# Kernel tuning notes

Hardware: AMD Instinct MI355X
Metric: run time of the kernel (lower is better)

The kernel has to match this reference:

```python
import jax, jax.numpy as jnp
import numpy as np

STATE_LEN = 128

def _layernorm(x, eps=1e-5):
    m = jnp.mean(x, axis=-1, keepdims=True)
    v = jnp.mean(jnp.square(x - m), axis=-1, keepdims=True)
    return (x - m) * jax.lax.rsqrt(v + eps)

def setup_inputs() -> dict:
    key = jax.random.key(0)
    ks = jax.random.split(key, 20)
    B, S, L = 2, 2048, STATE_LEN
    Din, Dk, Dv, H = 1024, 64, 64, 8
    T = S + 2 * L  # 2304
    x = jax.random.normal(ks[0], (B, T, Din), jnp.float32)
    def w(k, dout):
        return jax.random.normal(k, (H, Din, dout), jnp.float32) / np.sqrt(Din).astype(np.float32)
    inp = {
        'x': x,
        'ln_g':  1.0 + 0.02 * jax.random.normal(ks[1], (H, Din), jnp.float32),
        'ln_b':  0.02 * jax.random.normal(ks[2], (H, Din), jnp.float32),
        'ln_gs': 1.0 + 0.02 * jax.random.normal(ks[3], (H, Din), jnp.float32),
        'ln_bs': 0.02 * jax.random.normal(ks[4], (H, Din), jnp.float32),
        'ln_ge': 1.0 + 0.02 * jax.random.normal(ks[5], (H, Din), jnp.float32),
        'ln_be': 0.02 * jax.random.normal(ks[6], (H, Din), jnp.float32),
        'Wq':   w(ks[7], Dk),  'Wk':   w(ks[8], Dk),  'Wv':   w(ks[9], Dv),
        'Wq_s': w(ks[10], Dk), 'Wk_s': w(ks[11], Dk), 'Wv_s': w(ks[12], Dv),
        'Wq_e': w(ks[13], Dk), 'Wk_e': w(ks[14], Dk), 'Wv_e': w(ks[15], Dv),
        'offset': 0,
    }
    return inp

def _forward(x, ln_g, ln_b, ln_gs, ln_bs, ln_ge, ln_be,
             Wq, Wk, Wv, Wq_s, Wk_s, Wv_s, Wq_e, Wk_e, Wv_e):
    L = STATE_LEN
    B, T, Din = x.shape
    # extract_state: start state, middle sequence, end state
    xs, xm, xe = x[:, :L], x[:, L:T - L], x[:, T - L:]
    # LayerNorm stats are parameter-free; per-head affine applied after
    ns, nm, ne = _layernorm(xs), _layernorm(xm), _layernorm(xe)
    def aff(n, g, b):  # [B,seg,Din] -> [B,H,seg,Din]
        return n[:, None, :, :] * g[None, :, None, :] + b[None, :, None, :]
    hs, hm, he = aff(ns, ln_gs, ln_bs), aff(nm, ln_g, ln_b), aff(ne, ln_ge, ln_be)
    proj = lambda h, W: jnp.einsum('bhsd,hde->bhse', h, W)
    q = jnp.concatenate([proj(hs, Wq_s), proj(hm, Wq), proj(he, Wq_e)], axis=2)
    k = jnp.concatenate([proj(hs, Wk_s), proj(hm, Wk), proj(he, Wk_e)], axis=2)
    v = jnp.concatenate([proj(hs, Wv_s), proj(hm, Wv), proj(he, Wv_e)], axis=2)
    Dk = q.shape[-1]
    scores = jnp.einsum('bhsd,bhtd->bhst', q, k) / jnp.asarray(np.sqrt(Dk), q.dtype)
    # Faithful to the torch code: a FLOAT tril-of-ones mask is passed to SDPA,
    # which ADDS it to the scores (it does not set -inf anywhere).
    mask = jnp.tril(jnp.ones((T, T), scores.dtype))
    att = jax.nn.softmax(scores + mask, axis=-1)
    out = jnp.einsum('bhst,bhtd->bhsd', att, v)  # [B,H,T,Dv]
    H, Dv = out.shape[1], out.shape[3]
    # torch.concat over heads on last dim
    return out.transpose(0, 2, 1, 3).reshape(B, T, H * Dv)

def reference(x, ln_g, ln_b, ln_gs, ln_bs, ln_ge, ln_be,
              Wq, Wk, Wv, Wq_s, Wk_s, Wv_s, Wq_e, Wk_e, Wv_e, offset):
    # offset unused: position_embedders are None in this configuration
    return _forward(x, ln_g, ln_b, ln_gs, ln_bs, ln_ge, ln_be,
                    Wq, Wk, Wv, Wq_s, Wk_s, Wv_s, Wq_e, Wk_e, Wv_e)
```

## Files before the change

### kernel.cpp

```cpp
#include <hip/hip_runtime.h>

#define TSEQ 2304
#define DIN  1024
#define NH   8
#define DD   64
#define NC   1536
#define MROWS 4608
#define L2E  1.44269504f
#define EF   2.71828183f

typedef __attribute__((ext_vector_type(8))) short bf16x8;
typedef __attribute__((ext_vector_type(4))) float f32x4;
typedef __attribute__((ext_vector_type(4))) unsigned short u16x4;

__device__ __forceinline__ unsigned short f2bf(float f){
    union { float f; unsigned int u; } x; x.f = f;
    unsigned int r = x.u + 0x7FFFu + ((x.u >> 16) & 1u);
    return (unsigned short)(r >> 16);
}

__device__ __forceinline__ unsigned int pack_bf2(float a, float b){
    union { float f; unsigned int u; } xa, xb;
    xa.f = a; xb.f = b;
    return __builtin_amdgcn_perm(xb.u + 0x8000u, xa.u + 0x8000u, 0x07060302u);
}

__device__ __forceinline__ void gload_lds16(const void* g, void* l){
    __builtin_amdgcn_global_load_lds(
        (const __attribute__((address_space(1))) void*)g,
        (__attribute__((address_space(3))) void*)l, 16, 0, 0);
}

struct WArgs {
    const float* W[9];
    const float* g[3];
    const float* bv[3];
};

__global__ __launch_bounds__(256) void k_pre(WArgs a, const float* __restrict__ x,
                                             unsigned short* __restrict__ wb,
                                             float* __restrict__ bias,
                                             unsigned short* __restrict__ nrm)
{
    __shared__ float lds[64][65];
    __shared__ float red[4][64];
    __shared__ float r1[4], r2[4];
    const int bid = blockIdx.x;
    const int tid = threadIdx.x;
    if (bid < 1152){
        const int dt = bid & 15, h = (bid >> 4) & 7, sp = bid >> 7;
        const int seg = sp / 3, proj = sp % 3;
        const float* W = a.W[seg*3 + proj];
        const float* g = a.g[seg];
        const int d0 = dt * 64;
        {
            const int e = tid & 63, rq = tid >> 6;
#pragma unroll
            for (int rr = 0; rr < 16; ++rr){
                const int dl = rr*4 + rq;
                lds[dl][e] = W[((size_t)h*DIN + d0 + dl)*DD + e];
            }
        }
        __syncthreads();
        {
            const int dl = tid & 63, eq = tid >> 6;
            const int n0 = proj*512 + h*64;
            const float gv = g[h*DIN + d0 + dl];
#pragma unroll
            for (int rr = 0; rr < 16; ++rr){
                const int el = eq*16 + rr;
                wb[((size_t)seg*NC + n0 + el)*DIN + d0 + dl] = f2bf(lds[dl][el] * gv);
            }
        }
    } else if (bid < 1224){
        const int u = bid - 1152;
        const int h = u & 7, sp = u >> 3;
        const int seg = sp / 3, proj = sp % 3;
        const float* W  = a.W[seg*3 + proj];
        const float* bv = a.bv[seg];
        const int e = tid & 63, dc = tid >> 6;
        float sum = 0.f;
        for (int i = 0; i < 256; ++i){
            const int d = dc*256 + i;
            sum += bv[h*DIN + d] * W[((size_t)h*DIN + d)*DD + e];
        }
        red[dc][e] = sum;
        __syncthreads();
        if (dc == 0)
            bias[seg*NC + proj*512 + h*64 + e] = red[0][e] + red[1][e] + red[2][e] + red[3][e];
    } else {
        const int row = bid - 1224;
        const float* xr = x + (size_t)row * DIN;
        f32x4 v = *(const f32x4*)&xr[tid*4];
        float s1 = v[0]+v[1]+v[2]+v[3];
        float s2 = v[0]*v[0]+v[1]*v[1]+v[2]*v[2]+v[3]*v[3];
#pragma unroll
        for (int m = 1; m < 64; m <<= 1){ s1 += __shfl_xor(s1, m); s2 += __shfl_xor(s2, m); }
        const int wid = tid >> 6;
        if ((tid & 63) == 0){ r1[wid] = s1; r2[wid] = s2; }
        __syncthreads();
        s1 = r1[0]+r1[1]+r1[2]+r1[3];
        s2 = r2[0]+r2[1]+r2[2]+r2[3];
        const float mean = s1 * (1.f/1024.f);
        const float var  = s2 * (1.f/1024.f) - mean*mean;
        const float rstd = rsqrtf(var + 1e-5f);
        u16x4 ov;
#pragma unroll
        for (int j = 0; j < 4; ++j) ov[j] = f2bf((v[j]-mean)*rstd);
        *(u16x4*)&nrm[(size_t)row*DIN + tid*4] = ov;
    }
}

__global__ __launch_bounds__(256) void k_gemm(
    const unsigned short* __restrict__ A,
    const unsigned short* __restrict__ Wb,
    const float* __restrict__ bias,
    unsigned short* __restrict__ qo,
    unsigned short* __restrict__ ko,
    unsigned short* __restrict__ vt)
{
    __shared__ unsigned short As[128*32];
    __shared__ unsigned short Bs[128*32];
    const int mt = blockIdx.x, nt = blockIdx.y;
    const int row0 = mt*128, n0 = nt*128;
    const int rloc = row0 % TSEQ;
    const int seg = (rloc < 128) ? 0 : (rloc < 2176 ? 1 : 2);
    const unsigned short* Bp = Wb + (size_t)seg * NC * DIN;
    const int tid = threadIdx.x;
    const int wid = tid >> 6, lane = tid & 63;
    const int wr = wid >> 1, wc = wid & 1;
    const int lr = lane & 15, lg = lane >> 4;
    const int srow = lane >> 2;
    const int selem = (lane & 3) * 8;
    f32x4 acc[4][4];
#pragma unroll
    for (int m = 0; m < 4; ++m)
#pragma unroll
        for (int n = 0; n < 4; ++n) acc[m][n] = (f32x4){0.f,0.f,0.f,0.f};

    for (int kt = 0; kt < DIN/32; ++kt){
        const int k0 = kt*32;
        __syncthreads();
#pragma unroll
        for (int i = 0; i < 2; ++i){
            const int c = wid*2 + i;
            const int r = c*16 + srow;
            gload_lds16(&A [(size_t)(row0 + r)*DIN + k0 + selem], &As[c*512]);
            gload_lds16(&Bp[(size_t)(n0  + r)*DIN + k0 + selem], &Bs[c*512]);
        }
        __syncthreads();
        bf16x8 af[4], bfr[4];
#pragma unroll
        for (int m = 0; m < 4; ++m) af[m]  = *(const bf16x8*)&As[(wr*64 + m*16 + lr)*32 + lg*8];
#pragma unroll
        for (int n = 0; n < 4; ++n) bfr[n] = *(const bf16x8*)&Bs[(wc*64 + n*16 + lr)*32 + lg*8];
#pragma unroll
        for (int m = 0; m < 4; ++m)
#pragma unroll
            for (int n = 0; n < 4; ++n)
                acc[m][n] = __builtin_amdgcn_mfma_f32_16x16x32_bf16(af[m], bfr[n], acc[m][n], 0, 0, 0);
    }
    const int b_ = row0 / TSEQ;
    const int t0 = row0 - b_ * TSEQ;
#pragma unroll
    for (int m = 0; m < 4; ++m){
#pragma unroll
        for (int n = 0; n < 4; ++n){
            const int nglob = n0 + wc*64 + n*16 + lr;
            const float bs = bias[seg*NC + nglob];
            const int proj = nglob >> 9, hh = (nglob >> 6) & 7, e = nglob & 63;
            if (proj < 2){
                unsigned short* op = (proj == 0) ? qo : ko;
                const float scale = (proj == 0) ? 0.125f * L2E : 1.0f;
                const size_t ob = ((size_t)(b_*NH + hh) * TSEQ) * DD + e;
#pragma unroll
                for (int j = 0; j < 4; ++j){
                    const int t = t0 + wr*64 + m*16 + 4*lg + j;
                    op[ob + (size_t)t * DD] = f2bf((acc[m][n][j] + bs) * scale);
                }
            } else {
                unsigned short* vp = vt + ((size_t)(b_*NH + hh)*DD + e)*TSEQ;
                const int t = t0 + wr*64 + m*16 + 4*lg;
                u16x4 pk;
#pragma unroll
                for (int j = 0; j < 4; ++j) pk[j] = f2bf(acc[m][n][j] + bs);
                *(u16x4*)&vp[t] = pk;
            }
        }
    }
}

__global__ __launch_bounds__(256) void k_attn(
    const unsigned short* __restrict__ Q,
    const unsigned short* __restrict__ K,
    const unsigned short* __restrict__ Vt,
    float* __restrict__ po0,
    float* __restrict__ po1,
    float* __restrict__ out2,
    float* __restrict__ pl)
{
    __shared__ unsigned short Ks[2][64*64];
    __shared__ unsigned short Vs[2][64*64];
    __shared__ unsigned short Plds[4][16][72];
    const int qt = blockIdx.x;
    const int bh = blockIdx.y;
    const int z  = blockIdx.z;
    const int kt0 = z*12, kt1 = kt0 + 12;
    const int tid  = threadIdx.x;
    const int w    = tid >> 6;
    const int lane = tid & 63;
    const int lr = lane & 15, lg = lane >> 4;
    const size_t qkb = (size_t)bh * TSEQ * DD;
    const size_t vtb = (size_t)bh * DD * TSEQ;
    const int q0 = qt*64 + w*16;
    const int qr = q0 + lr;

    const int rsub = lane >> 3;
    const int cgx  = (lane & 7) ^ rsub;
    const char* Kbase  = (const char*)(K  + qkb);
    const char* Vtbase = (const char*)(Vt + vtb);

    bf16x8 aq[2];
#pragma unroll
    for (int ks = 0; ks < 2; ++ks)
        aq[ks] = *(const bf16x8*)&Q[qkb + (size_t)(q0 + lr)*DD + ks*32 + lg*8];

    float lsum = 0.f;
    f32x4 o[4];
#pragma unroll
    for (int nd = 0; nd < 4; ++nd) o[nd] = (f32x4){0.f,0.f,0.f,0.f};

    auto stage = [&](int kt, int b){
        const int kn = kt*64;
#pragma unroll
        for (int i = 0; i < 2; ++i){
            const int c = w*2 + i;
            const int r = c*8 + rsub;
            gload_lds16(Kbase  + (size_t)(kn + r)*128 + cgx*16,              &Ks[b][c*512]);
            gload_lds16(Vtbase + (size_t)r*(TSEQ*2) + (size_t)kn*2 + cgx*16, &Vs[b][c*512]);
        }
    };

    stage(kt0, 0);
    __syncthreads();

    unsigned int* PldsW = (unsigned int*)&Plds[w][0][0];

    int buf = 0;
    for (int kt = kt0; kt < kt1; ++kt){
        const int kc0 = kt*64;
        if (kt + 1 < kt1) stage(kt + 1, buf ^ 1);
        f32x4 s[4];
#pragma unroll
        for (int ns = 0; ns < 4; ++ns) s[ns] = (f32x4){0.f,0.f,0.f,0.f};
#pragma unroll
        for (int ks = 0; ks < 2; ++ks){
#pragma unroll
            for (int ns = 0; ns < 4; ++ns){
                bf16x8 bk = *(const bf16x8*)&Ks[buf][(ns*16 + lr)*64 + (((4*ks + lg) ^ (lr & 7))*8)];
                s[ns] = __builtin_amdgcn_mfma_f32_16x16x32_bf16(bk, aq[ks], s[ns], 0, 0, 0);
            }
        }
        if (kt == qt){
            lsum *= EF;
#pragma unroll
            for (int nd = 0; nd < 4; ++nd)
#pragma unroll
                for (int j = 0; j < 4; ++j) o[nd][j] *= EF;
#pragma unroll
            for (int ns = 0; ns < 4; ++ns){
                const int kb = kc0 + ns*16 + 4*lg;
                float p0 = exp2f(s[ns][0] + ((kb + 0 <= qr) ? L2E : 0.f));
                float p1 = exp2f(s[ns][1] + ((kb + 1 <= qr) ? L2E : 0.f));
                float p2 = exp2f(s[ns][2] + ((kb + 2 <= qr) ? L2E : 0.f));
                float p3 = exp2f(s[ns][3] + ((kb + 3 <= qr) ? L2E : 0.f));
                lsum += (p0 + p1) + (p2 + p3);
                PldsW[lr*36 + ns*8 + 2*lg + 0] = pack_bf2(p0, p1);
                PldsW[lr*36 + ns*8 + 2*lg + 1] = pack_bf2(p2, p3);
            }
        } else {
#pragma unroll
            for (int ns = 0; ns < 4; ++ns){
                float p0 = exp2f(s[ns][0]);
                float p1 = exp2f(s[ns][1]);
                float p2 = exp2f(s[ns][2]);
                float p3 = exp2f(s[ns][3]);
                lsum += (p0 + p1) + (p2 + p3);
                PldsW[lr*36 + ns*8 + 2*lg + 0] = pack_bf2(p0, p1);
                PldsW[lr*36 + ns*8 + 2*lg + 1] = pack_bf2(p2, p3);
            }
        }
#pragma unroll
        for (int ks = 0; ks < 2; ++ks){
            bf16x8 pa = *(const bf16x8*)&Plds[w][lr][ks*32 + lg*8];
#pragma unroll
            for (int nd = 0; nd < 4; ++nd){
                bf16x8 bv = *(const bf16x8*)&Vs[buf][(nd*16 + lr)*64 + (((4*ks + lg) ^ (lr & 7))*8)];
                o[nd] = __builtin_amdgcn_mfma_f32_16x16x32_bf16(pa, bv, o[nd], 0, 0, 0);
            }
        }
        __syncthreads();
        buf ^= 1;
    }
    if (qt >= kt1){
        lsum *= EF;
#pragma unroll
        for (int nd = 0; nd < 4; ++nd)
#pragma unroll
            for (int j = 0; j < 4; ++j) o[nd][j] *= EF;
    }
    lsum += __shfl_xor(lsum, 16);
    lsum += __shfl_xor(lsum, 32);
    const int tix = (z*16 + bh)*36 + qt;
    if (lg == 0) pl[tix*64 + w*16 + lr] = lsum;
    const int rowb = w*16 + 4*lg;
    if (z < 2){
        float* po = (z == 0) ? po0 : po1;
        const size_t tb = (size_t)(bh*36 + qt) * 4096;
#pragma unroll
        for (int j = 0; j < 4; ++j)
#pragma unroll
            for (int nd = 0; nd < 4; ++nd)
                po[tb + (size_t)(rowb + j)*64 + nd*16 + lr] = o[nd][j];
    } else {
        const int b_ = bh >> 3, hh = bh & 7;
#pragma unroll
        for (int j = 0; j < 4; ++j){
            const int t = qt*64 + rowb + j;
            const size_t ob = ((size_t)(b_*TSEQ + t))*512 + hh*64;
#pragma unroll
            for (int nd = 0; nd < 4; ++nd)
                out2[ob + nd*16 + lr] = o[nd][j];
        }
    }
}

__global__ __launch_bounds__(256) void k_comb(
    const float* __restrict__ po0, const float* __restrict__ po1,
    const float* __restrict__ pl, float* __restrict__ out)
{
    const int qt = blockIdx.x, bh = blockIdx.y;
    const int b_ = bh >> 3, hh = bh & 7;
    const int tid = threadIdx.x;
    const int row = tid >> 2;
    const int c0  = (tid & 3) * 16;
    const int t0ix = bh*36 + qt;
    const float inv = 1.0f / (pl[t0ix*64 + row] + pl[(576 + t0ix)*64 + row] + pl[(1152 + t0ix)*64 + row]);
    const size_t tb = (size_t)t0ix * 4096 + row*64 + c0;
    const size_t ob = ((size_t)b_*TSEQ + qt*64 + row)*512 + hh*64 + c0;
#pragma unroll
    for (int i = 0; i < 4; ++i){
        f32x4 a = *(const f32x4*)&po0[tb + i*4];
        f32x4 b = *(const f32x4*)&po1[tb + i*4];
        f32x4 c = *(const f32x4*)&out[ob + i*4];
        f32x4 r;
#pragma unroll
        for (int j = 0; j < 4; ++j) r[j] = (a[j] + b[j] + c[j]) * inv;
        *(f32x4*)&out[ob + i*4] = r;
    }
}

extern "C" void kernel_launch(void* const* d_in, const int* in_sizes, int n_in,
                              void* d_out, int out_size, void* d_ws, size_t ws_size,
                              hipStream_t stream)
{
    const float* x     = (const float*)d_in[0];
    const float* ln_g  = (const float*)d_in[1];
    const float* ln_b  = (const float*)d_in[2];
    const float* ln_gs = (const float*)d_in[3];
    const float* ln_bs = (const float*)d_in[4];
    const float* ln_ge = (const float*)d_in[5];
    const float* ln_be = (const float*)d_in[6];
    const float* Wq    = (const float*)d_in[7];
    const float* Wk    = (const float*)d_in[8];
    const float* Wv    = (const float*)d_in[9];
    const float* Wq_s  = (const float*)d_in[10];
    const float* Wk_s  = (const float*)d_in[11];
    const float* Wv_s  = (const float*)d_in[12];
    const float* Wq_e  = (const float*)d_in[13];
    const float* Wk_e  = (const float*)d_in[14];
    const float* Wv_e  = (const float*)d_in[15];

    uint8_t* w = (uint8_t*)d_ws;
    unsigned short* nrm = (unsigned short*)(w);
    unsigned short* wb  = (unsigned short*)(w + 9437184);
    float*          bia = (float*)        (w + 18874368);
    unsigned short* q_  = (unsigned short*)(w + 18892800);
    unsigned short* k_  = (unsigned short*)(w + 23611392);
    unsigned short* vt_ = (unsigned short*)(w + 28329984);
    float*          pl  = (float*)        (w + 33048576);
    float*          po0 = (float*)        (w);
    float*          po1 = (float*)        (w + 9437184);

    WArgs wa;
    wa.W[0] = Wq_s; wa.W[1] = Wk_s; wa.W[2] = Wv_s;
    wa.W[3] = Wq;   wa.W[4] = Wk;   wa.W[5] = Wv;
    wa.W[6] = Wq_e; wa.W[7] = Wk_e; wa.W[8] = Wv_e;
    wa.g[0] = ln_gs; wa.g[1] = ln_g; wa.g[2] = ln_ge;
    wa.bv[0] = ln_bs; wa.bv[1] = ln_b; wa.bv[2] = ln_be;

    float* out = (float*)d_out;
    k_pre <<<dim3(5832),      dim3(256), 0, stream>>>(wa, x, wb, bia, nrm);
    k_gemm<<<dim3(36, 12),    dim3(256), 0, stream>>>(nrm, wb, bia, q_, k_, vt_);
    k_attn<<<dim3(36, 16, 3), dim3(256), 0, stream>>>(q_, k_, vt_, po0, po1, out, pl);
    k_comb<<<dim3(36, 16),    dim3(256), 0, stream>>>(po0, po1, pl, out);
}
```

Measured before the change: 109.9 us.

## Double query rows per wave, split keys four ways, combine partials via atomics

Each wave now handles 32 query rows instead of 16, so every K/V tile loaded into LDS is reused across twice as many queries. The key range is split into four chunks of 9 tiles instead of three of 12. Partial outputs are accumulated straight into the zeroed output with float atomicAdd rather than through separate partial buffers, leaving only a per-row normalisation pass. The P packing uses the hardware v_cvt_pk_bf16_f32 instruction. In exchange the change adds a memset, atomic traffic, extra register pressure and a non-deterministic summation order.

```diff
diff --git a/kernel.cpp b/kernel.cpp
--- a/kernel.cpp
+++ b/kernel.cpp
@@ -19,10 +19,10 @@
     return (unsigned short)(r >> 16);
 }
 
-__device__ __forceinline__ unsigned int pack_bf2(float a, float b){
-    union { float f; unsigned int u; } xa, xb;
-    xa.f = a; xb.f = b;
-    return __builtin_amdgcn_perm(xb.u + 0x8000u, xa.u + 0x8000u, 0x07060302u);
+__device__ __forceinline__ unsigned int cvtpk(float a, float b){
+    unsigned int r;
+    asm("v_cvt_pk_bf16_f32 %0, %1, %2" : "=v"(r) : "v"(a), "v"(b));
+    return r;
 }
 
 __device__ __forceinline__ void gload_lds16(const void* g, void* l){
@@ -194,41 +194,43 @@
     const unsigned short* __restrict__ Q,
     const unsigned short* __restrict__ K,
     const unsigned short* __restrict__ Vt,
-    float* __restrict__ po0,
-    float* __restrict__ po1,
-    float* __restrict__ out2,
+    float* __restrict__ out,
     float* __restrict__ pl)
 {
     __shared__ unsigned short Ks[2][64*64];
     __shared__ unsigned short Vs[2][64*64];
-    __shared__ unsigned short Plds[4][16][72];
-    const int qt = blockIdx.x;
-    const int bh = blockIdx.y;
-    const int z  = blockIdx.z;
-    const int kt0 = z*12, kt1 = kt0 + 12;
+    __shared__ unsigned short Plds[4][32][72];
+    const int qtb = blockIdx.x;
+    const int bh  = blockIdx.y;
+    const int z   = blockIdx.z;
+    const int kt0 = z*9, kt1 = kt0 + 9;
     const int tid  = threadIdx.x;
     const int w    = tid >> 6;
     const int lane = tid & 63;
     const int lr = lane & 15, lg = lane >> 4;
     const size_t qkb = (size_t)bh * TSEQ * DD;
     const size_t vtb = (size_t)bh * DD * TSEQ;
-    const int q0 = qt*64 + w*16;
-    const int qr = q0 + lr;
+    const int q0w = qtb*128 + w*32;
+    const int kd  = qtb*2 + (w >> 1);
 
     const int rsub = lane >> 3;
     const int cgx  = (lane & 7) ^ rsub;
     const char* Kbase  = (const char*)(K  + qkb);
     const char* Vtbase = (const char*)(Vt + vtb);
 
-    bf16x8 aq[2];
-#pragma unroll
-    for (int ks = 0; ks < 2; ++ks)
-        aq[ks] = *(const bf16x8*)&Q[qkb + (size_t)(q0 + lr)*DD + ks*32 + lg*8];
-
-    float lsum = 0.f;
-    f32x4 o[4];
-#pragma unroll
-    for (int nd = 0; nd < 4; ++nd) o[nd] = (f32x4){0.f,0.f,0.f,0.f};
+    bf16x8 aq[2][2];
+#pragma unroll
+    for (int qg = 0; qg < 2; ++qg)
+#pragma unroll
+        for (int ks = 0; ks < 2; ++ks)
+            aq[qg][ks] = *(const bf16x8*)&Q[qkb + (size_t)(q0w + qg*16 + lr)*DD + ks*32 + lg*8];
+
+    float lsum[2] = {0.f, 0.f};
+    f32x4 o[2][4];
+#pragma unroll
+    for (int qg = 0; qg < 2; ++qg)
+#pragma unroll
+        for (int nd = 0; nd < 4; ++nd) o[qg][nd] = (f32x4){0.f,0.f,0.f,0.f};
 
     auto stage = [&](int kt, int b){
         const int kn = kt*64;
@@ -250,113 +252,134 @@
     for (int kt = kt0; kt < kt1; ++kt){
         const int kc0 = kt*64;
         if (kt + 1 < kt1) stage(kt + 1, buf ^ 1);
-        f32x4 s[4];
-#pragma unroll
-        for (int ns = 0; ns < 4; ++ns) s[ns] = (f32x4){0.f,0.f,0.f,0.f};
-#pragma unroll
-        for (int ks = 0; ks < 2; ++ks){
-#pragma unroll
-            for (int ns = 0; ns < 4; ++ns){
-                bf16x8 bk = *(const bf16x8*)&Ks[buf][(ns*16 + lr)*64 + (((4*ks + lg) ^ (lr & 7))*8)];
-                s[ns] = __builtin_amdgcn_mfma_f32_16x16x32_bf16(bk, aq[ks], s[ns], 0, 0, 0);
-            }
-        }
-        if (kt == qt){
-            lsum *= EF;
+        bf16x8 bk[2][4];
+#pragma unroll
+        for (int ks = 0; ks < 2; ++ks)
+#pragma unroll
+            for (int ns = 0; ns < 4; ++ns)
+                bk[ks][ns] = *(const bf16x8*)&Ks[buf][(ns*16 + lr)*64 + (((4*ks + lg) ^ (lr & 7))*8)];
+        f32x4 s[2][4];
+#pragma unroll
+        for (int qg = 0; qg < 2; ++qg)
+#pragma unroll
+            for (int ns = 0; ns < 4; ++ns) s[qg][ns] = (f32x4){0.f,0.f,0.f,0.f};
+#pragma unroll
+        for (int qg = 0; qg < 2; ++qg)
+#pragma unroll
+            for (int ks = 0; ks < 2; ++ks)
+#pragma unroll
+                for (int ns = 0; ns < 4; ++ns)
+                    s[qg][ns] = __builtin_amdgcn_mfma_f32_16x16x32_bf16(bk[ks][ns], aq[qg][ks], s[qg][ns], 0, 0, 0);
+        if (kt == kd){
+#pragma unroll
+            for (int qg = 0; qg < 2; ++qg){
+                lsum[qg] *= EF;
+#pragma unroll
+                for (int nd = 0; nd < 4; ++nd)
+#pragma unroll
+                    for (int j = 0; j < 4; ++j) o[qg][nd][j] *= EF;
+                const int qr = q0w + qg*16 + lr;
+#pragma unroll
+                for (int ns = 0; ns < 4; ++ns){
+                    const int kb = kc0 + ns*16 + 4*lg;
+                    float p0 = exp2f(s[qg][ns][0] + ((kb + 0 <= qr) ? L2E : 0.f));
+                    float p1 = exp2f(s[qg][ns][1] + ((kb + 1 <= qr) ? L2E : 0.f));
+                    float p2 = exp2f(s[qg][ns][2] + ((kb + 2 <= qr) ? L2E : 0.f));
+                    float p3 = exp2f(s[qg][ns][3] + ((kb + 3 <= qr) ? L2E : 0.f));
+                    lsum[qg] += (p0 + p1) + (p2 + p3);
+                    PldsW[(qg*16 + lr)*36 + ns*8 + 2*lg + 0] = cvtpk(p0, p1);
+                    PldsW[(qg*16 + lr)*36 + ns*8 + 2*lg + 1] = cvtpk(p2, p3);
+                }
+            }
+        } else {
+#pragma unroll
+            for (int qg = 0; qg < 2; ++qg){
+#pragma unroll
+                for (int ns = 0; ns < 4; ++ns){
+                    float p0 = exp2f(s[qg][ns][0]);
+                    float p1 = exp2f(s[qg][ns][1]);
+                    float p2 = exp2f(s[qg][ns][2]);
+                    float p3 = exp2f(s[qg][ns][3]);
+                    lsum[qg] += (p0 + p1) + (p2 + p3);
+                    PldsW[(qg*16 + lr)*36 + ns*8 + 2*lg + 0] = cvtpk(p0, p1);
+                    PldsW[(qg*16 + lr)*36 + ns*8 + 2*lg + 1] = cvtpk(p2, p3);
+                }
+            }
+        }
+        bf16x8 bv[2][4];
+#pragma unroll
+        for (int ks = 0; ks < 2; ++ks)
 #pragma unroll
             for (int nd = 0; nd < 4; ++nd)
-#pragma unroll
-                for (int j = 0; j < 4; ++j) o[nd][j] *= EF;
-#pragma unroll
-            for (int ns = 0; ns < 4; ++ns){
-                const int kb = kc0 + ns*16 + 4*lg;
-                float p0 = exp2f(s[ns][0] + ((kb + 0 <= qr) ? L2E : 0.f));
-                float p1 = exp2f(s[ns][1] + ((kb + 1 <= qr) ? L2E : 0.f));
-                float p2 = exp2f(s[ns][2] + ((kb + 2 <= qr) ? L2E : 0.f));
-                float p3 = exp2f(s[ns][3] + ((kb + 3 <= qr) ? L2E : 0.f));
-                lsum += (p0 + p1) + (p2 + p3);
-                PldsW[lr*36 + ns*8 + 2*lg + 0] = pack_bf2(p0, p1);
-                PldsW[lr*36 + ns*8 + 2*lg + 1] = pack_bf2(p2, p3);
-            }
-        } else {
-#pragma unroll
-            for (int ns = 0; ns < 4; ++ns){
-                float p0 = exp2f(s[ns][0]);
-                float p1 = exp2f(s[ns][1]);
-                float p2 = exp2f(s[ns][2]);
-                float p3 = exp2f(s[ns][3]);
-                lsum += (p0 + p1) + (p2 + p3);
-                PldsW[lr*36 + ns*8 + 2*lg + 0] = pack_bf2(p0, p1);
-                PldsW[lr*36 + ns*8 + 2*lg + 1] = pack_bf2(p2, p3);
-            }
-        }
-#pragma unroll
-        for (int ks = 0; ks < 2; ++ks){
-            bf16x8 pa = *(const bf16x8*)&Plds[w][lr][ks*32 + lg*8];
+                bv[ks][nd] = *(const bf16x8*)&Vs[buf][(nd*16 + lr)*64 + (((4*ks + lg) ^ (lr & 7))*8)];
+#pragma unroll
+        for (int qg = 0; qg < 2; ++qg){
+            bf16x8 pa0 = *(const bf16x8*)&Plds[w][qg*16 + lr][0*32 + lg*8];
+            bf16x8 pa1 = *(const bf16x8*)&Plds[w][qg*16 + lr][1*32 + lg*8];
 #pragma unroll
             for (int nd = 0; nd < 4; ++nd){
-                bf16x8 bv = *(const bf16x8*)&Vs[buf][(nd*16 + lr)*64 + (((4*ks + lg) ^ (lr & 7))*8)];
-                o[nd] = __builtin_amdgcn_mfma_f32_16x16x32_bf16(pa, bv, o[nd], 0, 0, 0);
+                o[qg][nd] = __builtin_amdgcn_mfma_f32_16x16x32_bf16(pa0, bv[0][nd], o[qg][nd], 0, 0, 0);
+                o[qg][nd] = __builtin_amdgcn_mfma_f32_16x16x32_bf16(pa1, bv[1][nd], o[qg][nd], 0, 0, 0);
             }
         }
         __syncthreads();
         buf ^= 1;
     }
-    if (qt >= kt1){
-        lsum *= EF;
-#pragma unroll
-        for (int nd = 0; nd < 4; ++nd)
-#pragma unroll
-            for (int j = 0; j < 4; ++j) o[nd][j] *= EF;
-    }
-    lsum += __shfl_xor(lsum, 16);
-    lsum += __shfl_xor(lsum, 32);
-    const int tix = (z*16 + bh)*36 + qt;
-    if (lg == 0) pl[tix*64 + w*16 + lr] = lsum;
-    const int rowb = w*16 + 4*lg;
-    if (z < 2){
-        float* po = (z == 0) ? po0 : po1;
-        const size_t tb = (size_t)(bh*36 + qt) * 4096;
-#pragma unroll
-        for (int j = 0; j < 4; ++j)
+    if (kd >= kt1){
+#pragma unroll
+        for (int qg = 0; qg < 2; ++qg){
+            lsum[qg] *= EF;
 #pragma unroll
             for (int nd = 0; nd < 4; ++nd)
-                po[tb + (size_t)(rowb + j)*64 + nd*16 + lr] = o[nd][j];
-    } else {
-        const int b_ = bh >> 3, hh = bh & 7;
+#pragma unroll
+                for (int j = 0; j < 4; ++j) o[qg][nd][j] *= EF;
+        }
+    }
+#pragma unroll
+    for (int qg = 0; qg < 2; ++qg){
+        lsum[qg] += __shfl_xor(lsum[qg], 16);
+        lsum[qg] += __shfl_xor(lsum[qg], 32);
+    }
+    const int pbase = ((z*16 + bh)*18 + qtb)*128 + w*32;
+    if (lg == 0){
+        pl[pbase + 0*16 + lr] = lsum[0];
+        pl[pbase + 1*16 + lr] = lsum[1];
+    }
+    const int b_ = bh >> 3, hh = bh & 7;
+#pragma unroll
+    for (int qg = 0; qg < 2; ++qg){
 #pragma unroll
         for (int j = 0; j < 4; ++j){
-            const int t = qt*64 + rowb + j;
+            const int t = q0w + qg*16 + 4*lg + j;
             const size_t ob = ((size_t)(b_*TSEQ + t))*512 + hh*64;
 #pragma unroll
             for (int nd = 0; nd < 4; ++nd)
-                out2[ob + nd*16 + lr] = o[nd][j];
-        }
-    }
-}
-
-__global__ __launch_bounds__(256) void k_comb(
-    const float* __restrict__ po0, const float* __restrict__ po1,
-    const float* __restrict__ pl, float* __restrict__ out)
+                atomicAdd(&out[ob + nd*16 + lr], o[qg][nd][j]);
+        }
+    }
+}
+
+__global__ __launch_bounds__(256) void k_norm(const float* __restrict__ pl, float* __restrict__ out)
 {
     const int qt = blockIdx.x, bh = blockIdx.y;
     const int b_ = bh >> 3, hh = bh & 7;
     const int tid = threadIdx.x;
     const int row = tid >> 2;
     const int c0  = (tid & 3) * 16;
-    const int t0ix = bh*36 + qt;
-    const float inv = 1.0f / (pl[t0ix*64 + row] + pl[(576 + t0ix)*64 + row] + pl[(1152 + t0ix)*64 + row]);
-    const size_t tb = (size_t)t0ix * 4096 + row*64 + c0;
-    const size_t ob = ((size_t)b_*TSEQ + qt*64 + row)*512 + hh*64 + c0;
+    const int t128  = qt >> 1;
+    const int rowin = (qt & 1)*64 + row;
+    float l = 0.f;
+#pragma unroll
+    for (int z = 0; z < 4; ++z)
+        l += pl[((z*16 + bh)*18 + t128)*128 + rowin];
+    const float inv = 1.0f / l;
+    const size_t ob = ((size_t)(b_*TSEQ + qt*64 + row))*512 + hh*64 + c0;
 #pragma unroll
     for (int i = 0; i < 4; ++i){
-        f32x4 a = *(const f32x4*)&po0[tb + i*4];
-        f32x4 b = *(const f32x4*)&po1[tb + i*4];
-        f32x4 c = *(const f32x4*)&out[ob + i*4];
-        f32x4 r;
-#pragma unroll
-        for (int j = 0; j < 4; ++j) r[j] = (a[j] + b[j] + c[j]) * inv;
-        *(f32x4*)&out[ob + i*4] = r;
+        f32x4 v = *(const f32x4*)&out[ob + i*4];
+#pragma unroll
+        for (int j = 0; j < 4; ++j) v[j] *= inv;
+        *(f32x4*)&out[ob + i*4] = v;
     }
 }
 
@@ -389,8 +412,6 @@
     unsigned short* k_  = (unsigned short*)(w + 23611392);
     unsigned short* vt_ = (unsigned short*)(w + 28329984);
     float*          pl  = (float*)        (w + 33048576);
-    float*          po0 = (float*)        (w);
-    float*          po1 = (float*)        (w + 9437184);
 
     WArgs wa;
     wa.W[0] = Wq_s; wa.W[1] = Wk_s; wa.W[2] = Wv_s;
@@ -400,8 +421,9 @@
     wa.bv[0] = ln_bs; wa.bv[1] = ln_b; wa.bv[2] = ln_be;
 
     float* out = (float*)d_out;
+    hipMemsetAsync(out, 0, (size_t)out_size * sizeof(float), stream);
     k_pre <<<dim3(5832),      dim3(256), 0, stream>>>(wa, x, wb, bia, nrm);
     k_gemm<<<dim3(36, 12),    dim3(256), 0, stream>>>(nrm, wb, bia, q_, k_, vt_);
-    k_attn<<<dim3(36, 16, 3), dim3(256), 0, stream>>>(q_, k_, vt_, po0, po1, out, pl);
-    k_comb<<<dim3(36, 16),    dim3(256), 0, stream>>>(po0, po1, pl, out);
-}
+    k_attn<<<dim3(18, 16, 4), dim3(256), 0, stream>>>(q_, k_, vt_, out, pl);
+    k_norm<<<dim3(36, 16),    dim3(256), 0, stream>>>(pl, out);
+}
```

Measured after the change: 127.5 us. 1.16x slower.
